# Optimization experiments

Hardware: AMD Instinct MI355X
Metric: run time of the kernel (lower is better)

Reference implementation:

```python
import jax, jax.numpy as jnp
import numpy as np

N_FFT = 1024
HOP = 256
N_MELS = 80
SR = 16000
N_ITER = 32
MOMENTUM = 0.99
B, T = 8, 1024


def _mel_filterbank(sr, n_fft, n_mels):
    # librosa.filters.mel (htk=False, norm='slaney') reimplemented in numpy
    f_sp = 200.0 / 3
    min_log_hz = 1000.0
    min_log_mel = min_log_hz / f_sp
    logstep = np.log(6.4) / 27.0

    def hz_to_mel(f):
        f = np.asarray(f, dtype=np.float64)
        return np.where(f >= min_log_hz,
                        min_log_mel + np.log(np.maximum(f, 1e-10) / min_log_hz) / logstep,
                        f / f_sp)

    def mel_to_hz(m):
        m = np.asarray(m, dtype=np.float64)
        return np.where(m >= min_log_mel,
                        min_log_hz * np.exp(logstep * (m - min_log_mel)),
                        m * f_sp)

    fftfreqs = np.linspace(0.0, sr / 2.0, n_fft // 2 + 1)
    mel_f = mel_to_hz(np.linspace(hz_to_mel(0.0), hz_to_mel(sr / 2.0), n_mels + 2))
    fdiff = np.diff(mel_f)
    ramps = mel_f[:, None] - fftfreqs[None, :]
    lower = -ramps[:-2] / fdiff[:-1][:, None]
    upper = ramps[2:] / fdiff[1:][:, None]
    weights = np.maximum(0.0, np.minimum(lower, upper))
    enorm = 2.0 / (mel_f[2:n_mels + 2] - mel_f[:n_mels])  # slaney norm
    return (weights * enorm[:, None]).astype(np.float32)


def _hann(n):
    return (0.5 - 0.5 * jnp.cos(2.0 * jnp.pi * jnp.arange(n) / n)).astype(jnp.float32)


def _stft(x, window):
    # x: [B, L] real -> [B, n_fft//2+1, F] complex (center=True, reflect pad)
    pad = N_FFT // 2
    xp = jnp.pad(x, ((0, 0), (pad, pad)), mode='reflect')
    n_frames = 1 + (xp.shape[-1] - N_FFT) // HOP
    idx = jnp.arange(n_frames)[:, None] * HOP + jnp.arange(N_FFT)[None, :]
    frames = xp[:, idx] * window  # [B, F, n_fft]
    return jnp.fft.rfft(frames, axis=-1).transpose(0, 2, 1)


def _istft(S, window):
    # S: [B, n_fft//2+1, F] complex -> [B, hop*(F-1)] real (center=True)
    bsz, _, n_frames = S.shape
    frames = jnp.fft.irfft(S.transpose(0, 2, 1), n=N_FFT, axis=-1) * window  # [B,F,n_fft]
    out_len = N_FFT + HOP * (n_frames - 1)
    idx = (jnp.arange(n_frames)[:, None] * HOP + jnp.arange(N_FFT)[None, :]).ravel()
    y = jnp.zeros((bsz, out_len), frames.dtype).at[:, idx].add(frames.reshape(bsz, -1))
    wsq = jnp.zeros((out_len,), window.dtype).at[idx].add(jnp.tile(window ** 2, n_frames))
    y = y / jnp.maximum(wsq, 1e-8)
    pad = N_FFT // 2
    return y[:, pad:-pad]


def _griffin_lim(mag, angles0, window):
    # mag: [B, bins, F] real magnitude, angles0 in [0,1)
    Sc = mag.astype(jnp.complex64)
    angles = jnp.exp(2j * jnp.pi * angles0).astype(jnp.complex64)
    rebuilt = jnp.zeros_like(Sc)
    beta = MOMENTUM / (1.0 + MOMENTUM)

    def body(carry, _):
        ang, reb_prev = carry
        inv = _istft(Sc * ang, window)
        reb = _stft(inv, window)
        new_ang = reb - beta * reb_prev
        new_ang = new_ang / (jnp.abs(new_ang) + 1e-16)
        return (new_ang, reb), None

    (angles, _), _ = jax.lax.scan(body, (angles, rebuilt), None, length=N_ITER)
    return _istft(Sc * angles, window)


def setup_inputs() -> dict:
    key = jax.random.key(0)
    k1, k2 = jax.random.split(key)
    mel_spec = jax.random.normal(k1, (B, N_MELS, T), dtype=jnp.float32)
    mel_basis = _mel_filterbank(SR, N_FFT, N_MELS)          # [80, 513]
    mel_inverse = jnp.asarray(np.linalg.pinv(mel_basis))     # [513, 80]
    angles0 = jax.random.uniform(k2, (B, N_FFT // 2 + 1, T), dtype=jnp.float32)
    return {"mel_spec": mel_spec, "mel_inverse": mel_inverse, "angles0": angles0}


def reference(mel_spec, mel_inverse, angles0):
    window = _hann(N_FFT)
    # mel -> linear magnitude spectrogram; |spec * e^{i theta}| == |spec|
    spec = jnp.einsum('fm,bmt->bft', mel_inverse, jnp.exp(mel_spec))
    mag = jnp.abs(spec)
    audio = _griffin_lim(mag, angles0, window)  # [B, hop*(T-1)]
    return audio
```

## Files before the change

### kernel.cpp

```cpp
#include <hip/hip_runtime.h>
#include <math.h>

#define BATCH    8
#define NFFT     1024
#define HOPSZ    256
#define NBINS    513
#define SROW     516
#define TFRAMES  1024
#define NBLK     (BATCH * TFRAMES)
#define LOUT     261888
#define YLEN     262912
#define NITER    32
#define TT       16

#define LDSIDX(i) ((i) + ((i) >> 5))
#define LDSBUF    532

__device__ __forceinline__ void wsync() {
    __asm__ volatile("s_waitcnt lgkmcnt(0)" ::: "memory");
}

template <int SIGN>
__device__ __forceinline__ void dft8(const float xr[8], const float xi[8],
                                     float yr[8], float yi[8])
{
    const float r2 = 0.70710678118654752f;
    float Ar = xr[0] + xr[4], Ai = xi[0] + xi[4];
    float Br = xr[0] - xr[4], Bi = xi[0] - xi[4];
    float Cr = xr[2] + xr[6], Ci = xi[2] + xi[6];
    float Dr = xr[2] - xr[6], Di = xi[2] - xi[6];
    float E0r = Ar + Cr, E0i = Ai + Ci;
    float E2r = Ar - Cr, E2i = Ai - Ci;
    float E1r, E1i, E3r, E3i;
    if (SIGN < 0) { E1r = Br + Di; E1i = Bi - Dr; E3r = Br - Di; E3i = Bi + Dr; }
    else          { E1r = Br - Di; E1i = Bi + Dr; E3r = Br + Di; E3i = Bi - Dr; }
    float ar = xr[1] + xr[5], ai = xi[1] + xi[5];
    float br = xr[1] - xr[5], bi = xi[1] - xi[5];
    float cr = xr[3] + xr[7], ci = xi[3] + xi[7];
    float dr = xr[3] - xr[7], di = xi[3] - xi[7];
    float O0r = ar + cr, O0i = ai + ci;
    float O2r = ar - cr, O2i = ai - ci;
    float O1r, O1i, O3r, O3i;
    if (SIGN < 0) { O1r = br + di; O1i = bi - dr; O3r = br - di; O3i = bi + dr; }
    else          { O1r = br - di; O1i = bi + dr; O3r = br + di; O3i = bi - dr; }
    float t1r, t1i, t2r, t2i, t3r, t3i;
    if (SIGN < 0) {
        t1r = r2 * (O1r + O1i); t1i = r2 * (O1i - O1r);
        t2r = O2i;              t2i = -O2r;
        t3r = r2 * (O3i - O3r); t3i = -r2 * (O3r + O3i);
    } else {
        t1r = r2 * (O1r - O1i); t1i = r2 * (O1i + O1r);
        t2r = -O2i;             t2i = O2r;
        t3r = -r2 * (O3r + O3i); t3i = r2 * (O3r - O3i);
    }
    yr[0] = E0r + O0r; yi[0] = E0i + O0i;  yr[4] = E0r - O0r; yi[4] = E0i - O0i;
    yr[1] = E1r + t1r; yi[1] = E1i + t1i;  yr[5] = E1r - t1r; yi[5] = E1i - t1i;
    yr[2] = E2r + t2r; yi[2] = E2i + t2i;  yr[6] = E2r - t2r; yi[6] = E2i - t2i;
    yr[3] = E3r + t3r; yi[3] = E3i + t3i;  yr[7] = E3r - t3r; yi[7] = E3i - t3i;
}

template <int SIGN, int S>
__device__ __forceinline__ void stage_write(float* lre, float* lim,
                                            const float yr[8], const float yi[8],
                                            int lane, const float2* __restrict__ tw)
{
    const int q = lane & (S - 1);
    const int p = lane / S;
    const int e = p * S;
    const int base = q + 8 * S * p;
#pragma unroll
    for (int j = 0; j < 8; ++j) {
        float vr = yr[j], vi = yi[j];
        if (j > 0) {
            float2 w = tw[j * e];
            float wr = w.x, wi = (SIGN < 0) ? w.y : -w.y;
            float tr = vr * wr - vi * wi;
            vi = vr * wi + vi * wr;
            vr = tr;
        }
        int o = LDSIDX(base + S * j);
        lre[o] = vr; lim[o] = vi;
    }
}

__device__ __forceinline__ void stage_read(const float* lre, const float* lim,
                                           float xr[8], float xi[8], int lane)
{
#pragma unroll
    for (int j = 0; j < 8; ++j) {
        int o = LDSIDX(lane + 64 * j);
        xr[j] = lre[o]; xi[j] = lim[o];
    }
}

template <int SIGN>
__device__ __forceinline__ void fft512(float* lre, float* lim,
                                       float xr[8], float xi[8],
                                       float yr[8], float yi[8],
                                       int lane, const float2* __restrict__ tw)
{
    dft8<SIGN>(xr, xi, yr, yi);
    stage_write<SIGN, 1>(lre, lim, yr, yi, lane, tw);
    wsync();
    stage_read(lre, lim, xr, xi, lane);
    wsync();
    dft8<SIGN>(xr, xi, yr, yi);
    stage_write<SIGN, 8>(lre, lim, yr, yi, lane, tw);
    wsync();
    stage_read(lre, lim, xr, xi, lane);
    dft8<SIGN>(xr, xi, yr, yi);
}

template <int SIGN>
__device__ __forceinline__ void fft512_lds(float* lre, float* lim,
                                           float xr[8], float xi[8],
                                           float yr[8], float yi[8],
                                           int lane, const float2* __restrict__ tw)
{
    stage_read(lre, lim, xr, xi, lane);
    wsync();
    fft512<SIGN>(lre, lim, xr, xi, yr, yi, lane, tw);
}

__global__ void k_setup(float2* tw512, float2* twh, float* win, float* wscl,
                        const float* __restrict__ melinv, float* __restrict__ melinvT,
                        float* __restrict__ wsqinv)
{
    int idx = blockIdx.x * blockDim.x + threadIdx.x;
    if (idx < 512) {
        double t1 = -2.0 * M_PI * (double)idx / 512.0;
        tw512[idx] = make_float2((float)cos(t1), (float)sin(t1));
        double t2 = -2.0 * M_PI * (double)idx / 1024.0;
        twh[idx] = make_float2((float)cos(t2), (float)sin(t2));
    }
    if (idx < 1024) {
        double w = 0.5 - 0.5 * cos(2.0 * M_PI * (double)idx / 1024.0);
        win[idx]  = (float)w;
        wscl[idx] = (float)(w / 512.0);
    }
    if (idx < 80 * NBINS) {
        int m = idx / NBINS, k = idx - m * NBINS;
        melinvT[idx] = melinv[k * 80 + m];
    }
    if (idx < YLEN) {
        int t = idx;
        int fhi = t >> 8;
        int flo = fhi - 3; if (flo < 0) flo = 0;
        if (fhi > TFRAMES - 1) fhi = TFRAMES - 1;
        float acc = 0.f;
        for (int f = flo; f <= fhi; ++f) {
            int n = t - (f << 8);
            float w = (float)(0.5 - 0.5 * cos(2.0 * M_PI * (double)n / 1024.0));
            acc += w * w;
        }
        float m = acc > 1e-8f ? acc : 1e-8f;
        wsqinv[t] = 1.0f / m;
    }
}

__global__ __launch_bounds__(256) void k_specinit(const float* __restrict__ mel,
                                                  const float* __restrict__ melinvT,
                                                  const float* __restrict__ ang0,
                                                  float* __restrict__ mag,
                                                  float2* __restrict__ spec)
{
    int b = blockIdx.y;
    int t0 = blockIdx.x * TT;
    int tid = threadIdx.x;
    __shared__ float em[80 * TT];
    for (int i = tid; i < 80 * TT; i += 256) {
        int m = i >> 4, tt = i & (TT - 1);
        em[i] = expf(mel[((size_t)b * 80 + m) * 1024 + t0 + tt]);
    }
    __syncthreads();

#pragma unroll
    for (int pass = 0; pass < 3; ++pass) {
        int k;
        if (pass < 2) k = tid + 256 * pass;
        else { if (tid != 0) break; k = 512; }

        float acc[TT];
#pragma unroll
        for (int tt = 0; tt < TT; ++tt) acc[tt] = 0.f;
        for (int m = 0; m < 80; ++m) {
            float wv = melinvT[m * NBINS + k];
            const float4 e0 = *(const float4*)&em[m * TT + 0];
            const float4 e1 = *(const float4*)&em[m * TT + 4];
            const float4 e2 = *(const float4*)&em[m * TT + 8];
            const float4 e3 = *(const float4*)&em[m * TT + 12];
            acc[0]  = fmaf(wv, e0.x, acc[0]);  acc[1]  = fmaf(wv, e0.y, acc[1]);
            acc[2]  = fmaf(wv, e0.z, acc[2]);  acc[3]  = fmaf(wv, e0.w, acc[3]);
            acc[4]  = fmaf(wv, e1.x, acc[4]);  acc[5]  = fmaf(wv, e1.y, acc[5]);
            acc[6]  = fmaf(wv, e1.z, acc[6]);  acc[7]  = fmaf(wv, e1.w, acc[7]);
            acc[8]  = fmaf(wv, e2.x, acc[8]);  acc[9]  = fmaf(wv, e2.y, acc[9]);
            acc[10] = fmaf(wv, e2.z, acc[10]); acc[11] = fmaf(wv, e2.w, acc[11]);
            acc[12] = fmaf(wv, e3.x, acc[12]); acc[13] = fmaf(wv, e3.y, acc[13]);
            acc[14] = fmaf(wv, e3.z, acc[14]); acc[15] = fmaf(wv, e3.w, acc[15]);
        }
        const float* ap = ang0 + ((size_t)b * NBINS + k) * 1024 + t0;
        float av[TT];
        *(float4*)&av[0]  = *(const float4*)(ap);
        *(float4*)&av[4]  = *(const float4*)(ap + 4);
        *(float4*)&av[8]  = *(const float4*)(ap + 8);
        *(float4*)&av[12] = *(const float4*)(ap + 12);
#pragma unroll
        for (int tt = 0; tt < TT; ++tt) {
            float mg = fabsf(acc[tt]);
            float sn, cn;
            sincospif(2.0f * av[tt], &sn, &cn);
            size_t row = ((size_t)b * 1024 + (t0 + tt)) * SROW;
            mag[row + k] = mg;
            spec[row + k] = make_float2(mg * cn, mg * sn);
        }
    }
}

__global__ __launch_bounds__(256) void k_ifft(const float2* __restrict__ spec,
                                              const float2* __restrict__ tw512,
                                              const float2* __restrict__ twh,
                                              const float* __restrict__ wscl,
                                              float* __restrict__ frames)
{
    __shared__ float scr[4][2][LDSBUF];
    int tid = threadIdx.x;
    int w = tid >> 6, lane = tid & 63;
    int blk = blockIdx.x * 4 + w;
    size_t row = (size_t)blk * SROW;
    float* lre = scr[w][0];
    float* lim = scr[w][1];
    float xr[8], xi[8], yr[8], yi[8];
#pragma unroll
    for (int r = 0; r < 8; ++r) {
        int k = lane + 64 * r;
        float2 v1 = spec[row + k];
        float2 v2 = spec[row + 512 - k];
        if (k == 0) { v1.y = 0.f; v2.y = 0.f; }
        float Ar = 0.5f * (v1.x + v2.x), Ai = 0.5f * (v1.y - v2.y);
        float Sr = 0.5f * (v1.x - v2.x), Si = 0.5f * (v1.y + v2.y);
        float2 W = twh[k];
        float Xor = W.x * Sr + W.y * Si;
        float Xoi = W.x * Si - W.y * Sr;
        xr[r] = Ar - Xoi;
        xi[r] = Ai + Xor;
    }
    fft512<1>(lre, lim, xr, xi, yr, yi, lane, tw512);
    size_t frow = (size_t)blk * 1024;
#pragma unroll
    for (int j = 0; j < 8; ++j) {
        int m = lane + 64 * j;
        float2 ws = *(const float2*)&wscl[2 * m];
        float2 o;
        o.x = yr[j] * ws.x;
        o.y = yi[j] * ws.y;
        *(float2*)&frames[frow + 2 * m] = o;
    }
}

__global__ __launch_bounds__(256) void k_oa(const float* __restrict__ frames,
                                            const float* __restrict__ wsqinv,
                                            float* __restrict__ audioR)
{
    int t4 = (blockIdx.x * 256 + threadIdx.x) * 4;
    if (t4 >= YLEN) return;
    int b = blockIdx.y;
    const float* fb = frames + (size_t)b * (TFRAMES * 1024);
    int fhi = t4 >> 8;
    int flo = fhi - 3; if (flo < 0) flo = 0;
    if (fhi > TFRAMES - 1) fhi = TFRAMES - 1;
    float4 acc = make_float4(0.f, 0.f, 0.f, 0.f);
    for (int ff = flo; ff <= fhi; ++ff) {
        float4 v = *(const float4*)&fb[(size_t)ff * 1024 + (t4 - (ff << 8))];
        acc.x += v.x; acc.y += v.y; acc.z += v.z; acc.w += v.w;
    }
    float4 wq = *(const float4*)&wsqinv[t4];
    acc.x *= wq.x; acc.y *= wq.y; acc.z *= wq.z; acc.w *= wq.w;
    *(float4*)&audioR[(size_t)b * YLEN + t4] = acc;
}

__global__ __launch_bounds__(256) void k_fused(const float* __restrict__ audioR,
                                               const float* __restrict__ mag,
                                               const float2* __restrict__ tw512,
                                               const float2* __restrict__ twh,
                                               const float* __restrict__ win,
                                               const float* __restrict__ wscl,
                                               float2* __restrict__ rebprev,
                                               float* __restrict__ frames,
                                               float beta)
{
    __shared__ float scr[4][2][LDSBUF];
    int tid = threadIdx.x;
    int w = tid >> 6, lane = tid & 63;
    int blk = blockIdx.x * 4 + w;
    int b = blk >> 10;
    int f = blk & 1023;
    const float* ab = audioR + (size_t)b * YLEN;
    float* lre = scr[w][0];
    float* lim = scr[w][1];

    float xr[8], xi[8], yr[8], yi[8];
    if (f >= 2 && f <= 1021) {
        const float* src = ab + f * HOPSZ;
#pragma unroll
        for (int j = 0; j < 8; ++j) {
            int n0 = 2 * (lane + 64 * j);
            float2 s = *(const float2*)&src[n0];
            float2 w2 = *(const float2*)&win[n0];
            xr[j] = s.x * w2.x;
            xi[j] = s.y * w2.y;
        }
    } else {
#pragma unroll
        for (int j = 0; j < 8; ++j) {
            int n0 = 2 * (lane + 64 * j);
            int j0 = f * HOPSZ + n0 - 512;
            int ja = (j0 < 0) ? -j0 : ((j0 >= LOUT) ? 2 * LOUT - 2 - j0 : j0);
            int j1 = j0 + 1;
            int jb = (j1 < 0) ? -j1 : ((j1 >= LOUT) ? 2 * LOUT - 2 - j1 : j1);
            float s0 = ab[ja + 512];
            float s1 = ab[jb + 512];
            float2 w2 = *(const float2*)&win[n0];
            xr[j] = s0 * w2.x;
            xi[j] = s1 * w2.y;
        }
    }
    fft512<-1>(lre, lim, xr, xi, yr, yi, lane, tw512);

#pragma unroll
    for (int j = 0; j < 8; ++j) {
        int o = LDSIDX(lane + 64 * j);
        lre[o] = yr[j]; lim[o] = yi[j];
    }
    wsync();

    size_t row = (size_t)blk * SROW;
#pragma unroll
    for (int r = 0; r < 5; ++r) {
        int p;
        if (r < 4) p = lane + 64 * r;
        else { if (lane != 0) break; p = 256; }
        int pm = (512 - p) & 511;
        float Zkr = lre[LDSIDX(p)],  Zki = lim[LDSIDX(p)];
        float Zmr = lre[LDSIDX(pm)], Zmi = lim[LDSIDX(pm)];
        float Ar = 0.5f * (Zkr + Zmr), Ai = 0.5f * (Zki - Zmi);
        float Sr = 0.5f * (Zkr - Zmr), Si = 0.5f * (Zki + Zmi);
        float2 W1 = twh[p];
        float U1r = W1.x * Sr - W1.y * Si, U1i = W1.x * Si + W1.y * Sr;
        float Xpr = Ar + U1i, Xpi = Ai - U1r;
        float w2r, w2i;
        if (p == 0) { w2r = -1.f; w2i = 0.f; }
        else { float2 W2 = twh[512 - p]; w2r = W2.x; w2i = W2.y; }
        float U2r = -w2r * Sr - w2i * Si, U2i = w2r * Si - w2i * Sr;
        float Xqr = Ar + U2i, Xqi = -Ai - U2r;
        int q = 512 - p;
        float2 pv1 = rebprev[row + p];
        float2 pv2 = rebprev[row + q];
        float v1x = Xpr - beta * pv1.x, v1y = Xpi - beta * pv1.y;
        float v2x = Xqr - beta * pv2.x, v2y = Xqi - beta * pv2.y;
        float a1 = sqrtf(v1x * v1x + v1y * v1y) + 1e-16f;
        float a2 = sqrtf(v2x * v2x + v2y * v2y) + 1e-16f;
        float sc1 = mag[row + p] / a1;
        float sc2 = mag[row + q] / a2;
        float s1x = v1x * sc1, s1y = v1y * sc1;
        float s2x = v2x * sc2, s2y = v2y * sc2;
        rebprev[row + p] = make_float2(Xpr, Xpi);
        rebprev[row + q] = make_float2(Xqr, Xqi);
        float Apr = 0.5f * (s1x + s2x), Api = 0.5f * (s1y - s2y);
        float Spr = 0.5f * (s1x - s2x), Spi = 0.5f * (s1y + s2y);
        float Xor = W1.x * Spr + W1.y * Spi;
        float Xoi = W1.x * Spi - W1.y * Spr;
        lre[LDSIDX(p)] = Apr - Xoi;
        lim[LDSIDX(p)] = Api + Xor;
        if (p > 0) {
            float Yor = -w2r * Spr + w2i * Spi;
            float Yoi =  w2r * Spi + w2i * Spr;
            lre[LDSIDX(512 - p)] = Apr - Yoi;
            lim[LDSIDX(512 - p)] = -Api + Yor;
        }
    }
    wsync();

    fft512_lds<1>(lre, lim, xr, xi, yr, yi, lane, tw512);
    size_t frow = (size_t)blk * 1024;
#pragma unroll
    for (int j = 0; j < 8; ++j) {
        int m = lane + 64 * j;
        float2 ws = *(const float2*)&wscl[2 * m];
        float2 o;
        o.x = yr[j] * ws.x;
        o.y = yi[j] * ws.y;
        *(float2*)&frames[frow + 2 * m] = o;
    }
}

__global__ __launch_bounds__(256) void k_gather(const float* __restrict__ frames,
                                                const float* __restrict__ wsqinv,
                                                float* __restrict__ out)
{
    int idx = (blockIdx.x * 256 + threadIdx.x) * 4;
    if (idx >= BATCH * LOUT) return;
    int b = idx / LOUT;
    int j = idx - b * LOUT;
    int t4 = j + 512;
    const float* fb = frames + (size_t)b * (TFRAMES * 1024);
    int fhi = t4 >> 8;
    int flo = fhi - 3; if (flo < 0) flo = 0;
    if (fhi > TFRAMES - 1) fhi = TFRAMES - 1;
    float4 acc = make_float4(0.f, 0.f, 0.f, 0.f);
    for (int ff = flo; ff <= fhi; ++ff) {
        float4 v = *(const float4*)&fb[(size_t)ff * 1024 + (t4 - (ff << 8))];
        acc.x += v.x; acc.y += v.y; acc.z += v.z; acc.w += v.w;
    }
    float4 wq = *(const float4*)&wsqinv[t4];
    acc.x *= wq.x; acc.y *= wq.y; acc.z *= wq.z; acc.w *= wq.w;
    *(float4*)&out[idx] = acc;
}

extern "C" void kernel_launch(void* const* d_in, const int* in_sizes, int n_in,
                              void* d_out, int out_size, void* d_ws, size_t ws_size,
                              hipStream_t stream)
{
    const float* mel    = (const float*)d_in[0];
    const float* melinv = (const float*)d_in[1];
    const float* ang0   = (const float*)d_in[2];
    float* out = (float*)d_out;

    char* ws = (char*)d_ws;
    size_t off = 0;
    auto carve = [&](size_t bytes) -> void* {
        void* p = ws + off;
        off += (bytes + 255) & ~(size_t)255;
        return p;
    };
    float2* tw512   = (float2*)carve(512 * sizeof(float2));
    float2* twh     = (float2*)carve(512 * sizeof(float2));
    float*  win     = (float*) carve(1024 * sizeof(float));
    float*  wscl    = (float*) carve(1024 * sizeof(float));
    float*  wsqinv  = (float*) carve((size_t)YLEN * sizeof(float));
    float*  melinvT = (float*) carve((size_t)80 * NBINS * sizeof(float));
    float*  mag     = (float*) carve((size_t)NBLK * SROW * sizeof(float));
    float2* spec    = (float2*)carve((size_t)NBLK * SROW * sizeof(float2));
    float2* rebp    = (float2*)carve((size_t)NBLK * SROW * sizeof(float2));
    float*  frames  = (float*) carve((size_t)NBLK * 1024 * sizeof(float));
    float*  audioR  = (float*) carve((size_t)BATCH * YLEN * sizeof(float));
    (void)ws_size; (void)in_sizes; (void)n_in; (void)out_size;

    const float beta = (float)(0.99 / 1.99);

    hipLaunchKernelGGL(k_setup, dim3((YLEN + 255) / 256), dim3(256), 0, stream,
                       tw512, twh, win, wscl, melinv, melinvT, wsqinv);
    hipLaunchKernelGGL(k_specinit, dim3(TFRAMES / TT, BATCH), dim3(256), 0, stream,
                       mel, melinvT, ang0, mag, spec);
    (void)hipMemsetAsync(rebp, 0, (size_t)NBLK * SROW * sizeof(float2), stream);

    hipLaunchKernelGGL(k_ifft, dim3(NBLK / 4), dim3(256), 0, stream,
                       spec, tw512, twh, wscl, frames);
    for (int it = 0; it < NITER; ++it) {
        hipLaunchKernelGGL(k_oa, dim3((YLEN / 4 + 255) / 256, BATCH), dim3(256), 0,
                           stream, frames, wsqinv, audioR);
        hipLaunchKernelGGL(k_fused, dim3(NBLK / 4), dim3(256), 0, stream,
                           audioR, mag, tw512, twh, win, wscl, rebp, frames, beta);
    }
    hipLaunchKernelGGL(k_gather, dim3(BATCH * LOUT / 4 / 256), dim3(256), 0, stream,
                       frames, wsqinv, out);
}
```

Baseline: 1.254 ms.

## Fuse overlap-add into STFT kernel via four-quarter frame buffers

Each iFFT frame is now written into one of four sample-aligned quarter buffers, so overlap-add becomes four strided contiguous loads summed inside the fused kernel. This removes the separate per-iteration overlap-add launch and its audio buffer round trip, and the two quarter sets are ping-ponged across iterations. The rebprev memset is dropped by passing beta=0 on the first iteration. The specinit time-tile is also halved. Edge regions are zeroed once up front. In exchange, every frame sample is read four times inside the fused kernel.

```diff
diff --git a/kernel.cpp b/kernel.cpp
--- a/kernel.cpp
+++ b/kernel.cpp
@@ -11,7 +11,9 @@
 #define LOUT     261888
 #define YLEN     262912
 #define NITER    32
-#define TT       16
+#define TT       8
+
+#define QS       ((size_t)BATCH * YLEN)
 
 #define LDSIDX(i) ((i) + ((i) >> 5))
 #define LDSBUF    532
@@ -122,6 +124,47 @@
     fft512<SIGN>(lre, lim, xr, xi, yr, yi, lane, tw);
 }
 
+__device__ __forceinline__ void write_qframe(float* __restrict__ Qout, int b, int f,
+                                             const float yr[8], const float yi[8],
+                                             const float* __restrict__ wscl, int lane)
+{
+    size_t base = (size_t)b * YLEN + (size_t)f * HOPSZ;
+#pragma unroll
+    for (int j = 0; j < 8; ++j) {
+        int n = 2 * (lane + 64 * j);
+        float2 ws = *(const float2*)&wscl[n];
+        float2 o;
+        o.x = yr[j] * ws.x;
+        o.y = yi[j] * ws.y;
+        *(float2*)&Qout[(size_t)(j >> 1) * QS + base + n] = o;
+    }
+}
+
+__device__ __forceinline__ float oa_q1(const float* __restrict__ Qin, int b, int t,
+                                       const float* __restrict__ wsqinv)
+{
+    const float* p = Qin + (size_t)b * YLEN + t;
+    float a = p[3 * QS];
+    a += p[2 * QS];
+    a += p[QS];
+    a += p[0];
+    return a * wsqinv[t];
+}
+
+__device__ __forceinline__ float2 oa_q2(const float* __restrict__ Qin, int b, int t,
+                                        const float* __restrict__ wsqinv)
+{
+    const float* p = Qin + (size_t)b * YLEN + t;
+    float2 a = *(const float2*)&p[3 * QS];
+    float2 v;
+    v = *(const float2*)&p[2 * QS]; a.x += v.x; a.y += v.y;
+    v = *(const float2*)&p[QS];     a.x += v.x; a.y += v.y;
+    v = *(const float2*)&p[0];      a.x += v.x; a.y += v.y;
+    float2 wq = *(const float2*)&wsqinv[t];
+    a.x *= wq.x; a.y *= wq.y;
+    return a;
+}
+
 __global__ void k_setup(float2* tw512, float2* twh, float* win, float* wscl,
                         const float* __restrict__ melinv, float* __restrict__ melinvT,
                         float* __restrict__ wsqinv)
@@ -158,6 +201,20 @@
     }
 }
 
+__global__ void k_zeroedges(float* qa, float* qb)
+{
+    int idx = blockIdx.x * 256 + threadIdx.x;
+    if (idx >= 49152) return;
+    float* buf = (idx < 24576) ? qa : qb;
+    int r = idx & 24575;
+    int k = r / 6144;
+    int r2 = r - k * 6144;
+    int b = r2 / 768;
+    int e = r2 - b * 768;
+    int t = (e < 256 * k) ? e : (262144 + e);
+    buf[(size_t)k * QS + (size_t)b * YLEN + t] = 0.f;
+}
+
 __global__ __launch_bounds__(256) void k_specinit(const float* __restrict__ mel,
                                                   const float* __restrict__ melinvT,
                                                   const float* __restrict__ ang0,
@@ -169,7 +226,7 @@
     int tid = threadIdx.x;
     __shared__ float em[80 * TT];
     for (int i = tid; i < 80 * TT; i += 256) {
-        int m = i >> 4, tt = i & (TT - 1);
+        int m = i >> 3, tt = i & (TT - 1);
         em[i] = expf(mel[((size_t)b * 80 + m) * 1024 + t0 + tt]);
     }
     __syncthreads();
@@ -187,23 +244,15 @@
             float wv = melinvT[m * NBINS + k];
             const float4 e0 = *(const float4*)&em[m * TT + 0];
             const float4 e1 = *(const float4*)&em[m * TT + 4];
-            const float4 e2 = *(const float4*)&em[m * TT + 8];
-            const float4 e3 = *(const float4*)&em[m * TT + 12];
-            acc[0]  = fmaf(wv, e0.x, acc[0]);  acc[1]  = fmaf(wv, e0.y, acc[1]);
-            acc[2]  = fmaf(wv, e0.z, acc[2]);  acc[3]  = fmaf(wv, e0.w, acc[3]);
-            acc[4]  = fmaf(wv, e1.x, acc[4]);  acc[5]  = fmaf(wv, e1.y, acc[5]);
-            acc[6]  = fmaf(wv, e1.z, acc[6]);  acc[7]  = fmaf(wv, e1.w, acc[7]);
-            acc[8]  = fmaf(wv, e2.x, acc[8]);  acc[9]  = fmaf(wv, e2.y, acc[9]);
-            acc[10] = fmaf(wv, e2.z, acc[10]); acc[11] = fmaf(wv, e2.w, acc[11]);
-            acc[12] = fmaf(wv, e3.x, acc[12]); acc[13] = fmaf(wv, e3.y, acc[13]);
-            acc[14] = fmaf(wv, e3.z, acc[14]); acc[15] = fmaf(wv, e3.w, acc[15]);
+            acc[0] = fmaf(wv, e0.x, acc[0]);  acc[1] = fmaf(wv, e0.y, acc[1]);
+            acc[2] = fmaf(wv, e0.z, acc[2]);  acc[3] = fmaf(wv, e0.w, acc[3]);
+            acc[4] = fmaf(wv, e1.x, acc[4]);  acc[5] = fmaf(wv, e1.y, acc[5]);
+            acc[6] = fmaf(wv, e1.z, acc[6]);  acc[7] = fmaf(wv, e1.w, acc[7]);
         }
         const float* ap = ang0 + ((size_t)b * NBINS + k) * 1024 + t0;
         float av[TT];
-        *(float4*)&av[0]  = *(const float4*)(ap);
-        *(float4*)&av[4]  = *(const float4*)(ap + 4);
-        *(float4*)&av[8]  = *(const float4*)(ap + 8);
-        *(float4*)&av[12] = *(const float4*)(ap + 12);
+        *(float4*)&av[0] = *(const float4*)(ap);
+        *(float4*)&av[4] = *(const float4*)(ap + 4);
 #pragma unroll
         for (int tt = 0; tt < TT; ++tt) {
             float mg = fabsf(acc[tt]);
@@ -220,7 +269,7 @@
                                               const float2* __restrict__ tw512,
                                               const float2* __restrict__ twh,
                                               const float* __restrict__ wscl,
-                                              float* __restrict__ frames)
+                                              float* __restrict__ Qout)
 {
     __shared__ float scr[4][2][LDSBUF];
     int tid = threadIdx.x;
@@ -245,47 +294,18 @@
         xi[r] = Ai + Xor;
     }
     fft512<1>(lre, lim, xr, xi, yr, yi, lane, tw512);
-    size_t frow = (size_t)blk * 1024;
-#pragma unroll
-    for (int j = 0; j < 8; ++j) {
-        int m = lane + 64 * j;
-        float2 ws = *(const float2*)&wscl[2 * m];
-        float2 o;
-        o.x = yr[j] * ws.x;
-        o.y = yi[j] * ws.y;
-        *(float2*)&frames[frow + 2 * m] = o;
-    }
-}
-
-__global__ __launch_bounds__(256) void k_oa(const float* __restrict__ frames,
-                                            const float* __restrict__ wsqinv,
-                                            float* __restrict__ audioR)
-{
-    int t4 = (blockIdx.x * 256 + threadIdx.x) * 4;
-    if (t4 >= YLEN) return;
-    int b = blockIdx.y;
-    const float* fb = frames + (size_t)b * (TFRAMES * 1024);
-    int fhi = t4 >> 8;
-    int flo = fhi - 3; if (flo < 0) flo = 0;
-    if (fhi > TFRAMES - 1) fhi = TFRAMES - 1;
-    float4 acc = make_float4(0.f, 0.f, 0.f, 0.f);
-    for (int ff = flo; ff <= fhi; ++ff) {
-        float4 v = *(const float4*)&fb[(size_t)ff * 1024 + (t4 - (ff << 8))];
-        acc.x += v.x; acc.y += v.y; acc.z += v.z; acc.w += v.w;
-    }
-    float4 wq = *(const float4*)&wsqinv[t4];
-    acc.x *= wq.x; acc.y *= wq.y; acc.z *= wq.z; acc.w *= wq.w;
-    *(float4*)&audioR[(size_t)b * YLEN + t4] = acc;
-}
-
-__global__ __launch_bounds__(256) void k_fused(const float* __restrict__ audioR,
+    write_qframe(Qout, blk >> 10, blk & 1023, yr, yi, wscl, lane);
+}
+
+__global__ __launch_bounds__(256) void k_fused(const float* __restrict__ Qin,
                                                const float* __restrict__ mag,
                                                const float2* __restrict__ tw512,
                                                const float2* __restrict__ twh,
                                                const float* __restrict__ win,
                                                const float* __restrict__ wscl,
+                                               const float* __restrict__ wsqinv,
                                                float2* __restrict__ rebprev,
-                                               float* __restrict__ frames,
+                                               float* __restrict__ Qout,
                                                float beta)
 {
     __shared__ float scr[4][2][LDSBUF];
@@ -294,17 +314,16 @@
     int blk = blockIdx.x * 4 + w;
     int b = blk >> 10;
     int f = blk & 1023;
-    const float* ab = audioR + (size_t)b * YLEN;
     float* lre = scr[w][0];
     float* lim = scr[w][1];
 
     float xr[8], xi[8], yr[8], yi[8];
     if (f >= 2 && f <= 1021) {
-        const float* src = ab + f * HOPSZ;
+        int tbase = f * HOPSZ;
 #pragma unroll
         for (int j = 0; j < 8; ++j) {
             int n0 = 2 * (lane + 64 * j);
-            float2 s = *(const float2*)&src[n0];
+            float2 s = oa_q2(Qin, b, tbase + n0, wsqinv);
             float2 w2 = *(const float2*)&win[n0];
             xr[j] = s.x * w2.x;
             xi[j] = s.y * w2.y;
@@ -317,8 +336,8 @@
             int ja = (j0 < 0) ? -j0 : ((j0 >= LOUT) ? 2 * LOUT - 2 - j0 : j0);
             int j1 = j0 + 1;
             int jb = (j1 < 0) ? -j1 : ((j1 >= LOUT) ? 2 * LOUT - 2 - j1 : j1);
-            float s0 = ab[ja + 512];
-            float s1 = ab[jb + 512];
+            float s0 = oa_q1(Qin, b, ja + 512, wsqinv);
+            float s1 = oa_q1(Qin, b, jb + 512, wsqinv);
             float2 w2 = *(const float2*)&win[n0];
             xr[j] = s0 * w2.x;
             xi[j] = s1 * w2.y;
@@ -381,39 +400,27 @@
     wsync();
 
     fft512_lds<1>(lre, lim, xr, xi, yr, yi, lane, tw512);
-    size_t frow = (size_t)blk * 1024;
-#pragma unroll
-    for (int j = 0; j < 8; ++j) {
-        int m = lane + 64 * j;
-        float2 ws = *(const float2*)&wscl[2 * m];
-        float2 o;
-        o.x = yr[j] * ws.x;
-        o.y = yi[j] * ws.y;
-        *(float2*)&frames[frow + 2 * m] = o;
-    }
-}
-
-__global__ __launch_bounds__(256) void k_gather(const float* __restrict__ frames,
-                                                const float* __restrict__ wsqinv,
-                                                float* __restrict__ out)
+    write_qframe(Qout, b, f, yr, yi, wscl, lane);
+}
+
+__global__ __launch_bounds__(256) void k_crop(const float* __restrict__ Qin,
+                                              const float* __restrict__ wsqinv,
+                                              float* __restrict__ out)
 {
     int idx = (blockIdx.x * 256 + threadIdx.x) * 4;
     if (idx >= BATCH * LOUT) return;
     int b = idx / LOUT;
     int j = idx - b * LOUT;
-    int t4 = j + 512;
-    const float* fb = frames + (size_t)b * (TFRAMES * 1024);
-    int fhi = t4 >> 8;
-    int flo = fhi - 3; if (flo < 0) flo = 0;
-    if (fhi > TFRAMES - 1) fhi = TFRAMES - 1;
-    float4 acc = make_float4(0.f, 0.f, 0.f, 0.f);
-    for (int ff = flo; ff <= fhi; ++ff) {
-        float4 v = *(const float4*)&fb[(size_t)ff * 1024 + (t4 - (ff << 8))];
-        acc.x += v.x; acc.y += v.y; acc.z += v.z; acc.w += v.w;
-    }
-    float4 wq = *(const float4*)&wsqinv[t4];
-    acc.x *= wq.x; acc.y *= wq.y; acc.z *= wq.z; acc.w *= wq.w;
-    *(float4*)&out[idx] = acc;
+    int t = j + 512;
+    const float* p = Qin + (size_t)b * YLEN + t;
+    float4 a = *(const float4*)&p[3 * QS];
+    float4 v;
+    v = *(const float4*)&p[2 * QS]; a.x += v.x; a.y += v.y; a.z += v.z; a.w += v.w;
+    v = *(const float4*)&p[QS];     a.x += v.x; a.y += v.y; a.z += v.z; a.w += v.w;
+    v = *(const float4*)&p[0];      a.x += v.x; a.y += v.y; a.z += v.z; a.w += v.w;
+    float4 wq = *(const float4*)&wsqinv[t];
+    a.x *= wq.x; a.y *= wq.y; a.z *= wq.z; a.w *= wq.w;
+    *(float4*)&out[idx] = a;
 }
 
 extern "C" void kernel_launch(void* const* d_in, const int* in_sizes, int n_in,
@@ -441,26 +448,27 @@
     float*  mag     = (float*) carve((size_t)NBLK * SROW * sizeof(float));
     float2* spec    = (float2*)carve((size_t)NBLK * SROW * sizeof(float2));
     float2* rebp    = (float2*)carve((size_t)NBLK * SROW * sizeof(float2));
-    float*  frames  = (float*) carve((size_t)NBLK * 1024 * sizeof(float));
-    float*  audioR  = (float*) carve((size_t)BATCH * YLEN * sizeof(float));
+    float*  QA      = (float*) carve(4 * QS * sizeof(float));
+    float*  QB      = (float*) carve(4 * QS * sizeof(float));
     (void)ws_size; (void)in_sizes; (void)n_in; (void)out_size;
 
     const float beta = (float)(0.99 / 1.99);
 
     hipLaunchKernelGGL(k_setup, dim3((YLEN + 255) / 256), dim3(256), 0, stream,
                        tw512, twh, win, wscl, melinv, melinvT, wsqinv);
+    hipLaunchKernelGGL(k_zeroedges, dim3(192), dim3(256), 0, stream, QA, QB);
     hipLaunchKernelGGL(k_specinit, dim3(TFRAMES / TT, BATCH), dim3(256), 0, stream,
                        mel, melinvT, ang0, mag, spec);
-    (void)hipMemsetAsync(rebp, 0, (size_t)NBLK * SROW * sizeof(float2), stream);
 
     hipLaunchKernelGGL(k_ifft, dim3(NBLK / 4), dim3(256), 0, stream,
-                       spec, tw512, twh, wscl, frames);
+                       spec, tw512, twh, wscl, QA);
     for (int it = 0; it < NITER; ++it) {
-        hipLaunchKernelGGL(k_oa, dim3((YLEN / 4 + 255) / 256, BATCH), dim3(256), 0,
-                           stream, frames, wsqinv, audioR);
+        const float* qin = (it & 1) ? QB : QA;
+        float*       qot = (it & 1) ? QA : QB;
+        float b_it = (it == 0) ? 0.f : beta;
         hipLaunchKernelGGL(k_fused, dim3(NBLK / 4), dim3(256), 0, stream,
-                           audioR, mag, tw512, twh, win, wscl, rebp, frames, beta);
-    }
-    hipLaunchKernelGGL(k_gather, dim3(BATCH * LOUT / 4 / 256), dim3(256), 0, stream,
-                       frames, wsqinv, out);
-}
+                           qin, mag, tw512, twh, win, wscl, wsqinv, rebp, qot, b_it);
+    }
+    hipLaunchKernelGGL(k_crop, dim3(BATCH * LOUT / 4 / 256), dim3(256), 0, stream,
+                       QA, wsqinv, out);
+}
```

After: 1.312 ms. +4.6%, slower.

## Recompute previous rebuilt spectrum by re-FFT of previous audio instead of storing it

Applied to the files above, without the earlier changes.

Removes the rebprev complex-spectrum buffer, which was read and written every iteration. Instead the kernel keeps the previous iteration's overlap-added audio in a ping-pong buffer and recomputes the previous STFT frame in-kernel with an extra FFT. This trades roughly 16 bytes per bin of global traffic per iteration for a second 512-point FFT per frame plus one read of a 4 KB audio window. It also halves TT in the init kernel, a separate tuning knob.

```diff
diff --git a/kernel.cpp b/kernel.cpp
--- a/kernel.cpp
+++ b/kernel.cpp
@@ -11,7 +11,7 @@
 #define LOUT     261888
 #define YLEN     262912
 #define NITER    32
-#define TT       16
+#define TT       8
 
 #define LDSIDX(i) ((i) + ((i) >> 5))
 #define LDSBUF    532
@@ -122,6 +122,58 @@
     fft512<SIGN>(lre, lim, xr, xi, yr, yi, lane, tw);
 }
 
+__device__ __forceinline__ void load_window(const float* __restrict__ ab, int f,
+                                            const float* __restrict__ win,
+                                            float xr[8], float xi[8], int lane)
+{
+    if (f >= 2 && f <= 1021) {
+        const float* src = ab + f * HOPSZ;
+#pragma unroll
+        for (int j = 0; j < 8; ++j) {
+            int n0 = 2 * (lane + 64 * j);
+            float2 s = *(const float2*)&src[n0];
+            float2 w2 = *(const float2*)&win[n0];
+            xr[j] = s.x * w2.x;
+            xi[j] = s.y * w2.y;
+        }
+    } else {
+#pragma unroll
+        for (int j = 0; j < 8; ++j) {
+            int n0 = 2 * (lane + 64 * j);
+            int j0 = f * HOPSZ + n0 - 512;
+            int ja = (j0 < 0) ? -j0 : ((j0 >= LOUT) ? 2 * LOUT - 2 - j0 : j0);
+            int j1 = j0 + 1;
+            int jb = (j1 < 0) ? -j1 : ((j1 >= LOUT) ? 2 * LOUT - 2 - j1 : j1);
+            float s0 = ab[ja + 512];
+            float s1 = ab[jb + 512];
+            float2 w2 = *(const float2*)&win[n0];
+            xr[j] = s0 * w2.x;
+            xi[j] = s1 * w2.y;
+        }
+    }
+}
+
+__device__ __forceinline__ void posttwist_pair(const float* lre, const float* lim,
+                                               const float2* __restrict__ twh,
+                                               int p,
+                                               float& Xpr, float& Xpi,
+                                               float& Xqr, float& Xqi)
+{
+    int pm = (512 - p) & 511;
+    float Zkr = lre[LDSIDX(p)],  Zki = lim[LDSIDX(p)];
+    float Zmr = lre[LDSIDX(pm)], Zmi = lim[LDSIDX(pm)];
+    float Ar = 0.5f * (Zkr + Zmr), Ai = 0.5f * (Zki - Zmi);
+    float Sr = 0.5f * (Zkr - Zmr), Si = 0.5f * (Zki + Zmi);
+    float2 W1 = twh[p];
+    float U1r = W1.x * Sr - W1.y * Si, U1i = W1.x * Si + W1.y * Sr;
+    Xpr = Ar + U1i; Xpi = Ai - U1r;
+    float w2r, w2i;
+    if (p == 0) { w2r = -1.f; w2i = 0.f; }
+    else { float2 W2 = twh[512 - p]; w2r = W2.x; w2i = W2.y; }
+    float U2r = -w2r * Sr - w2i * Si, U2i = w2r * Si - w2i * Sr;
+    Xqr = Ar + U2i; Xqi = -Ai - U2r;
+}
+
 __global__ void k_setup(float2* tw512, float2* twh, float* win, float* wscl,
                         const float* __restrict__ melinv, float* __restrict__ melinvT,
                         float* __restrict__ wsqinv)
@@ -169,7 +221,7 @@
     int tid = threadIdx.x;
     __shared__ float em[80 * TT];
     for (int i = tid; i < 80 * TT; i += 256) {
-        int m = i >> 4, tt = i & (TT - 1);
+        int m = i >> 3, tt = i & (TT - 1);
         em[i] = expf(mel[((size_t)b * 80 + m) * 1024 + t0 + tt]);
     }
     __syncthreads();
@@ -187,23 +239,15 @@
             float wv = melinvT[m * NBINS + k];
             const float4 e0 = *(const float4*)&em[m * TT + 0];
             const float4 e1 = *(const float4*)&em[m * TT + 4];
-            const float4 e2 = *(const float4*)&em[m * TT + 8];
-            const float4 e3 = *(const float4*)&em[m * TT + 12];
-            acc[0]  = fmaf(wv, e0.x, acc[0]);  acc[1]  = fmaf(wv, e0.y, acc[1]);
-            acc[2]  = fmaf(wv, e0.z, acc[2]);  acc[3]  = fmaf(wv, e0.w, acc[3]);
-            acc[4]  = fmaf(wv, e1.x, acc[4]);  acc[5]  = fmaf(wv, e1.y, acc[5]);
-            acc[6]  = fmaf(wv, e1.z, acc[6]);  acc[7]  = fmaf(wv, e1.w, acc[7]);
-            acc[8]  = fmaf(wv, e2.x, acc[8]);  acc[9]  = fmaf(wv, e2.y, acc[9]);
-            acc[10] = fmaf(wv, e2.z, acc[10]); acc[11] = fmaf(wv, e2.w, acc[11]);
-            acc[12] = fmaf(wv, e3.x, acc[12]); acc[13] = fmaf(wv, e3.y, acc[13]);
-            acc[14] = fmaf(wv, e3.z, acc[14]); acc[15] = fmaf(wv, e3.w, acc[15]);
+            acc[0] = fmaf(wv, e0.x, acc[0]);  acc[1] = fmaf(wv, e0.y, acc[1]);
+            acc[2] = fmaf(wv, e0.z, acc[2]);  acc[3] = fmaf(wv, e0.w, acc[3]);
+            acc[4] = fmaf(wv, e1.x, acc[4]);  acc[5] = fmaf(wv, e1.y, acc[5]);
+            acc[6] = fmaf(wv, e1.z, acc[6]);  acc[7] = fmaf(wv, e1.w, acc[7]);
         }
         const float* ap = ang0 + ((size_t)b * NBINS + k) * 1024 + t0;
         float av[TT];
-        *(float4*)&av[0]  = *(const float4*)(ap);
-        *(float4*)&av[4]  = *(const float4*)(ap + 4);
-        *(float4*)&av[8]  = *(const float4*)(ap + 8);
-        *(float4*)&av[12] = *(const float4*)(ap + 12);
+        *(float4*)&av[0] = *(const float4*)(ap);
+        *(float4*)&av[4] = *(const float4*)(ap + 4);
 #pragma unroll
         for (int tt = 0; tt < TT; ++tt) {
             float mg = fabsf(acc[tt]);
@@ -278,13 +322,13 @@
     *(float4*)&audioR[(size_t)b * YLEN + t4] = acc;
 }
 
-__global__ __launch_bounds__(256) void k_fused(const float* __restrict__ audioR,
+__global__ __launch_bounds__(256) void k_fused(const float* __restrict__ audioCur,
+                                               const float* __restrict__ audioPrev,
                                                const float* __restrict__ mag,
                                                const float2* __restrict__ tw512,
                                                const float2* __restrict__ twh,
                                                const float* __restrict__ win,
                                                const float* __restrict__ wscl,
-                                               float2* __restrict__ rebprev,
                                                float* __restrict__ frames,
                                                float beta)
 {
@@ -294,38 +338,41 @@
     int blk = blockIdx.x * 4 + w;
     int b = blk >> 10;
     int f = blk & 1023;
-    const float* ab = audioR + (size_t)b * YLEN;
     float* lre = scr[w][0];
     float* lim = scr[w][1];
-
     float xr[8], xi[8], yr[8], yi[8];
-    if (f >= 2 && f <= 1021) {
-        const float* src = ab + f * HOPSZ;
+
+    float xpPr[4], xpPi[4], xqPr[4], xqPi[4];
+    float xcPr = 0.f, xcPi = 0.f;
+    if (beta != 0.f) {
+        const float* abp = audioPrev + (size_t)b * YLEN;
+        load_window(abp, f, win, xr, xi, lane);
+        fft512<-1>(lre, lim, xr, xi, yr, yi, lane, tw512);
 #pragma unroll
         for (int j = 0; j < 8; ++j) {
-            int n0 = 2 * (lane + 64 * j);
-            float2 s = *(const float2*)&src[n0];
-            float2 w2 = *(const float2*)&win[n0];
-            xr[j] = s.x * w2.x;
-            xi[j] = s.y * w2.y;
-        }
+            int o = LDSIDX(lane + 64 * j);
+            lre[o] = yr[j]; lim[o] = yi[j];
+        }
+        wsync();
+#pragma unroll
+        for (int r = 0; r < 4; ++r)
+            posttwist_pair(lre, lim, twh, lane + 64 * r,
+                           xpPr[r], xpPi[r], xqPr[r], xqPi[r]);
+        if (lane == 0) {
+            xcPr = lre[LDSIDX(256)];
+            xcPi = -lim[LDSIDX(256)];
+        }
+        wsync();
     } else {
 #pragma unroll
-        for (int j = 0; j < 8; ++j) {
-            int n0 = 2 * (lane + 64 * j);
-            int j0 = f * HOPSZ + n0 - 512;
-            int ja = (j0 < 0) ? -j0 : ((j0 >= LOUT) ? 2 * LOUT - 2 - j0 : j0);
-            int j1 = j0 + 1;
-            int jb = (j1 < 0) ? -j1 : ((j1 >= LOUT) ? 2 * LOUT - 2 - j1 : j1);
-            float s0 = ab[ja + 512];
-            float s1 = ab[jb + 512];
-            float2 w2 = *(const float2*)&win[n0];
-            xr[j] = s0 * w2.x;
-            xi[j] = s1 * w2.y;
-        }
-    }
+        for (int r = 0; r < 4; ++r) {
+            xpPr[r] = 0.f; xpPi[r] = 0.f; xqPr[r] = 0.f; xqPi[r] = 0.f;
+        }
+    }
+
+    const float* ab = audioCur + (size_t)b * YLEN;
+    load_window(ab, f, win, xr, xi, lane);
     fft512<-1>(lre, lim, xr, xi, yr, yi, lane, tw512);
-
 #pragma unroll
     for (int j = 0; j < 8; ++j) {
         int o = LDSIDX(lane + 64 * j);
@@ -335,36 +382,23 @@
 
     size_t row = (size_t)blk * SROW;
 #pragma unroll
-    for (int r = 0; r < 5; ++r) {
-        int p;
-        if (r < 4) p = lane + 64 * r;
-        else { if (lane != 0) break; p = 256; }
-        int pm = (512 - p) & 511;
-        float Zkr = lre[LDSIDX(p)],  Zki = lim[LDSIDX(p)];
-        float Zmr = lre[LDSIDX(pm)], Zmi = lim[LDSIDX(pm)];
-        float Ar = 0.5f * (Zkr + Zmr), Ai = 0.5f * (Zki - Zmi);
-        float Sr = 0.5f * (Zkr - Zmr), Si = 0.5f * (Zki + Zmi);
+    for (int r = 0; r < 4; ++r) {
+        int p = lane + 64 * r;
+        int q = 512 - p;
+        float Xpr, Xpi, Xqr, Xqi;
+        posttwist_pair(lre, lim, twh, p, Xpr, Xpi, Xqr, Xqi);
         float2 W1 = twh[p];
-        float U1r = W1.x * Sr - W1.y * Si, U1i = W1.x * Si + W1.y * Sr;
-        float Xpr = Ar + U1i, Xpi = Ai - U1r;
         float w2r, w2i;
         if (p == 0) { w2r = -1.f; w2i = 0.f; }
         else { float2 W2 = twh[512 - p]; w2r = W2.x; w2i = W2.y; }
-        float U2r = -w2r * Sr - w2i * Si, U2i = w2r * Si - w2i * Sr;
-        float Xqr = Ar + U2i, Xqi = -Ai - U2r;
-        int q = 512 - p;
-        float2 pv1 = rebprev[row + p];
-        float2 pv2 = rebprev[row + q];
-        float v1x = Xpr - beta * pv1.x, v1y = Xpi - beta * pv1.y;
-        float v2x = Xqr - beta * pv2.x, v2y = Xqi - beta * pv2.y;
+        float v1x = Xpr - beta * xpPr[r], v1y = Xpi - beta * xpPi[r];
+        float v2x = Xqr - beta * xqPr[r], v2y = Xqi - beta * xqPi[r];
         float a1 = sqrtf(v1x * v1x + v1y * v1y) + 1e-16f;
         float a2 = sqrtf(v2x * v2x + v2y * v2y) + 1e-16f;
         float sc1 = mag[row + p] / a1;
         float sc2 = mag[row + q] / a2;
         float s1x = v1x * sc1, s1y = v1y * sc1;
         float s2x = v2x * sc2, s2y = v2y * sc2;
-        rebprev[row + p] = make_float2(Xpr, Xpi);
-        rebprev[row + q] = make_float2(Xqr, Xqi);
         float Apr = 0.5f * (s1x + s2x), Api = 0.5f * (s1y - s2y);
         float Spr = 0.5f * (s1x - s2x), Spi = 0.5f * (s1y + s2y);
         float Xor = W1.x * Spr + W1.y * Spi;
@@ -377,6 +411,15 @@
             lre[LDSIDX(512 - p)] = Apr - Yoi;
             lim[LDSIDX(512 - p)] = -Api + Yor;
         }
+    }
+    if (lane == 0) {
+        float Zr = lre[LDSIDX(256)], Zi = lim[LDSIDX(256)];
+        float Xr = Zr, Xi = -Zi;
+        float vx = Xr - beta * xcPr, vy = Xi - beta * xcPi;
+        float a = sqrtf(vx * vx + vy * vy) + 1e-16f;
+        float sc = mag[row + 256] / a;
+        lre[LDSIDX(256)] = vx * sc;
+        lim[LDSIDX(256)] = -(vy * sc);
     }
     wsync();
 
@@ -440,9 +483,9 @@
     float*  melinvT = (float*) carve((size_t)80 * NBINS * sizeof(float));
     float*  mag     = (float*) carve((size_t)NBLK * SROW * sizeof(float));
     float2* spec    = (float2*)carve((size_t)NBLK * SROW * sizeof(float2));
-    float2* rebp    = (float2*)carve((size_t)NBLK * SROW * sizeof(float2));
     float*  frames  = (float*) carve((size_t)NBLK * 1024 * sizeof(float));
-    float*  audioR  = (float*) carve((size_t)BATCH * YLEN * sizeof(float));
+    float*  audioU  = (float*) carve((size_t)BATCH * YLEN * sizeof(float));
+    float*  audioV  = (float*) carve((size_t)BATCH * YLEN * sizeof(float));
     (void)ws_size; (void)in_sizes; (void)n_in; (void)out_size;
 
     const float beta = (float)(0.99 / 1.99);
@@ -451,15 +494,17 @@
                        tw512, twh, win, wscl, melinv, melinvT, wsqinv);
     hipLaunchKernelGGL(k_specinit, dim3(TFRAMES / TT, BATCH), dim3(256), 0, stream,
                        mel, melinvT, ang0, mag, spec);
-    (void)hipMemsetAsync(rebp, 0, (size_t)NBLK * SROW * sizeof(float2), stream);
 
     hipLaunchKernelGGL(k_ifft, dim3(NBLK / 4), dim3(256), 0, stream,
                        spec, tw512, twh, wscl, frames);
     for (int it = 0; it < NITER; ++it) {
+        float* cur  = (it & 1) ? audioV : audioU;
+        float* prev = (it & 1) ? audioU : audioV;
+        float b_it = (it == 0) ? 0.f : beta;
         hipLaunchKernelGGL(k_oa, dim3((YLEN / 4 + 255) / 256, BATCH), dim3(256), 0,
-                           stream, frames, wsqinv, audioR);
+                           stream, frames, wsqinv, cur);
         hipLaunchKernelGGL(k_fused, dim3(NBLK / 4), dim3(256), 0, stream,
-                           audioR, mag, tw512, twh, win, wscl, rebp, frames, beta);
+                           cur, prev, mag, tw512, twh, win, wscl, frames, b_it);
     }
     hipLaunchKernelGGL(k_gather, dim3(BATCH * LOUT / 4 / 256), dim3(256), 0, stream,
                        frames, wsqinv, out);
```

Result: slower. 1.418 ms (+13.1%).
